# Kernel tuning notes

Measured on AMD Instinct MI355X. Metric: run time of the kernel, lower is better.

Reference implementation:

```python
import math
import jax, jax.numpy as jnp
import numpy as np

EPS_ATTN = 1e-8
LN_EPS = 1e-5


def layer_norm(x, g, b):
    mu = jnp.mean(x, axis=-1, keepdims=True)
    var = jnp.var(x, axis=-1, keepdims=True)
    return (x - mu) * jax.lax.rsqrt(var + LN_EPS) * g + b


def setup_inputs() -> dict:
    key = jax.random.key(0)
    ks = jax.random.split(key, 12)
    b, n, dim = 8, 8192, 384
    emb = 384
    m = int(emb * 0.5)  # 192 random features
    s = 0.02
    x = jax.random.normal(ks[0], (b, n, dim), dtype=jnp.float32)
    # fixed random-feature matrix (orthogonal*sqrt(m) in torch; random gaussian suffices as a baseline param)
    w = jax.random.normal(ks[1], (m, emb), dtype=jnp.float32) * math.sqrt(m) / math.sqrt(emb)
    # linear weights stored as [in, out] (torch Linear applies x @ W.T + b)
    kqv_w = jax.random.normal(ks[2], (dim, 3 * emb), dtype=jnp.float32) * s
    kqv_b = jax.random.normal(ks[3], (3 * emb,), dtype=jnp.float32) * s
    proj_w = jax.random.normal(ks[4], (emb, emb), dtype=jnp.float32) * s
    proj_b = jax.random.normal(ks[5], (emb,), dtype=jnp.float32) * s
    ln1_g = 1.0 + jax.random.normal(ks[6], (dim,), dtype=jnp.float32) * s
    ln1_b = jax.random.normal(ks[7], (dim,), dtype=jnp.float32) * s
    ln2_g = 1.0 + jax.random.normal(ks[8], (emb,), dtype=jnp.float32) * s
    ln2_b = jax.random.normal(ks[9], (emb,), dtype=jnp.float32) * s
    mlp_w1 = jax.random.normal(ks[10], (emb, emb), dtype=jnp.float32) * s
    mlp_b1 = jnp.zeros((emb,), dtype=jnp.float32)
    mlp_w2 = jax.random.normal(ks[11], (emb, emb), dtype=jnp.float32) * s
    mlp_b2 = jnp.zeros((emb,), dtype=jnp.float32)
    return {"x": x, "w": w, "kqv_w": kqv_w, "kqv_b": kqv_b, "proj_w": proj_w,
            "proj_b": proj_b, "ln1_g": ln1_g, "ln1_b": ln1_b, "ln2_g": ln2_g,
            "ln2_b": ln2_b, "mlp_w1": mlp_w1, "mlp_b1": mlp_b1,
            "mlp_w2": mlp_w2, "mlp_b2": mlp_b2}


def prm_exp(x, w):
    # FAVOR+ positive random features: exp(w @ x - |x|^2/2) / sqrt(m)
    m = w.shape[0]
    xd = 0.5 * jnp.sum(x * x, axis=-1, keepdims=True)          # [b, t, 1]
    wtx = jnp.einsum('bti,mi->btm', x, w)                       # [b, t, m]
    return jnp.exp(wtx - xd) / math.sqrt(m)


def reference(x, w, kqv_w, kqv_b, proj_w, proj_b, ln1_g, ln1_b,
              ln2_g, ln2_b, mlp_w1, mlp_b1, mlp_w2, mlp_b2):
    emb = proj_w.shape[0]
    h = layer_norm(x, ln1_g, ln1_b)
    kqv = h @ kqv_w + kqv_b                                     # [b, n, 3*emb]
    k, q, v = jnp.split(kqv, 3, axis=-1)
    kp = prm_exp(k, w)                                          # [b, n, m]
    qp = prm_exp(q, w)                                          # [b, n, m]
    D = jnp.einsum('btm,bm->bt', qp, kp.sum(axis=1))[..., None] # [b, n, 1]
    kptv = jnp.einsum('btn,btm->bnm', v, kp)                    # [b, emb, m]
    y = jnp.einsum('btm,bnm->btn', qp, kptv) / (D + EPS_ATTN)   # [b, n, emb]
    y = v + (y @ proj_w + proj_b)                               # residual (dropout=0)
    h2 = layer_norm(y, ln2_g, ln2_b)
    mlp = jax.nn.gelu(h2 @ mlp_w1 + mlp_b1, approximate=False) @ mlp_w2 + mlp_b2
    return y + mlp
```

## Files before the change

kernel.cpp:

```cpp
#include <hip/hip_runtime.h>
#include <cstdint>
#include <cstddef>


typedef __attribute__((ext_vector_type(8))) short s16x8;
typedef __attribute__((ext_vector_type(4))) short s16x4;
typedef __attribute__((ext_vector_type(4))) float fx4;
typedef __attribute__((ext_vector_type(8))) float fx8;

__device__ __forceinline__ float bf2f(short s) {
  union { float f; unsigned u; } z; z.u = ((unsigned)(unsigned short)s) << 16; return z.f;
}
__device__ __forceinline__ short f2bf(float f) {
  union { float f; unsigned u; } z; z.f = f;
  unsigned u = z.u;
  u += 0x7fffu + ((u >> 16) & 1u);
  return (short)(u >> 16);
}

__device__ __forceinline__ void mfma_bf16(fx4& d, s16x8 a, s16x8 b) {
  asm("v_mfma_f32_16x16x32_bf16 %0, %1, %2, %0" : "+v"(d) : "v"(a), "v"(b));
}

enum : int { M_BIAS=1, M_EXP=2, M_DIV=4, M_RESID=8, M_GELU=16, M_TSTORE=32,
             M_BATCHBT=64, M_KQVT=128, M_RESIDT=256, M_F32OUT=512 };

template<int BM, int BN, int MODE>
__global__ __launch_bounds__(256)
void gemm_tn(const short* __restrict__ A, int lda,
             const short* __restrict__ Bt, int ldbt, long btStride,
             short* __restrict__ C, int ldc,
             int K,
             const float* __restrict__ bias,
             const float* __restrict__ rowvec, float escale,
             const short* __restrict__ resid, int ldr, int rcol,
             short* __restrict__ vt)
{
  constexpr int WM = BM / 2, WN = BN / 2, MR = WM / 16, NR = WN / 16;
  constexpr int AIT = BM * 8 / 256, BIT = BN * 8 / 256;
  __shared__ __align__(16) short Al[BM][64];
  __shared__ __align__(16) short Bl[BN][64];

  const int tid = threadIdx.x;
  const int gx = gridDim.x;
  const int nwg = gx * gridDim.y;
  const int o = blockIdx.x + gx * blockIdx.y;
  const int swz = (o & 7) * (nwg >> 3) + (o >> 3);
  const int bx = swz % gx, by = swz / gx;
  const int row0 = by * BM, col0 = bx * BN;

  const short* Bt2 = (MODE & M_BATCHBT)
      ? Bt + (size_t)(row0 >> 13) * (size_t)btStride : Bt;
  const int w = tid >> 6, l = tid & 63;
  const int wr = w >> 1, wc = w & 1;
  const int lr = l & 15, lk = l >> 4;

  fx4 acc[MR][NR];
#pragma unroll
  for (int m = 0; m < MR; ++m)
#pragma unroll
    for (int n = 0; n < NR; ++n)
#pragma unroll
      for (int j = 0; j < 4; ++j) acc[m][n][j] = 0.0f;

  s16x8 areg[AIT], breg[BIT];

  auto loadA = [&](int kt) {
    const short* p = A + (size_t)row0 * lda + kt * 64;
#pragma unroll
    for (int i = 0; i < AIT; ++i) {
      int ch = i * 256 + tid;
      areg[i] = *(const s16x8*)(p + (size_t)(ch >> 3) * lda + ((ch & 7) * 8));
    }
  };
  auto loadB = [&](int kt) {
    const short* p = Bt2 + (size_t)col0 * ldbt + kt * 64;
#pragma unroll
    for (int i = 0; i < BIT; ++i) {
      int ch = i * 256 + tid;
      breg[i] = *(const s16x8*)(p + (size_t)(ch >> 3) * ldbt + ((ch & 7) * 8));
    }
  };
  auto storeA = [&]() {
#pragma unroll
    for (int i = 0; i < AIT; ++i) {
      int ch = i * 256 + tid, row = ch >> 3;
      *(s16x8*)&Al[row][((ch ^ row) & 7) * 8] = areg[i];
    }
  };
  auto storeB = [&]() {
#pragma unroll
    for (int i = 0; i < BIT; ++i) {
      int ch = i * 256 + tid, row = ch >> 3;
      *(s16x8*)&Bl[row][((ch ^ row) & 7) * 8] = breg[i];
    }
  };

  const int NT = K / 64;
  loadA(0); loadB(0); storeA(); storeB();
  __syncthreads();
  for (int kt = 0; kt < NT; ++kt) {
    if (kt + 1 < NT) { loadA(kt + 1); loadB(kt + 1); }
#pragma unroll
    for (int kk = 0; kk < 2; ++kk) {
      s16x8 af[MR], bfr[NR];
#pragma unroll
      for (int m = 0; m < MR; ++m) {
        const int ar = wr * WM + m * 16 + lr;
        af[m] = *(const s16x8*)&Al[ar][(((kk * 4 + lk) ^ ar) & 7) * 8];
      }
#pragma unroll
      for (int n = 0; n < NR; ++n) {
        const int br = wc * WN + n * 16 + lr;
        bfr[n] = *(const s16x8*)&Bl[br][(((kk * 4 + lk) ^ br) & 7) * 8];
      }
#pragma unroll
      for (int m = 0; m < MR; ++m)
#pragma unroll
        for (int n = 0; n < NR; ++n)
          mfma_bf16(acc[m][n], af[m], bfr[n]);
    }
    if (kt + 1 < NT) {
      __syncthreads();
      storeA(); storeB();
      __syncthreads();
    }
  }

#pragma unroll
  for (int m = 0; m < MR; ++m) {
#pragma unroll
    for (int n = 0; n < NR; ++n) {
      const int gcol = col0 + wc * WN + n * 16 + lr;
      const float bv = (MODE & M_BIAS) ? bias[gcol] : 0.0f;
#pragma unroll
      for (int j = 0; j < 4; ++j) {
        const int grow = row0 + wr * WM + m * 16 + lk * 4 + j;
        float v = acc[m][n][j] + bv;
        if (MODE & M_EXP)  v = expf(v - rowvec[grow]) * escale;
        if (MODE & M_DIV)  v = v / (rowvec[grow] + 1e-8f);
        if (MODE & M_GELU) v = 0.5f * v * (1.0f + erff(v * 0.70710678118654752f));
        if (MODE & M_RESID)  v += bf2f(resid[(size_t)grow * ldr + rcol + gcol]);
        if (MODE & M_RESIDT) v += bf2f(resid[((size_t)((grow >> 13) * ldr + gcol)) * 8192 + (grow & 8191)]);
        if (MODE & M_F32OUT) {
          ((float*)C)[(size_t)grow * ldc + gcol] = v;
        } else if (MODE & M_TSTORE) {
          C[((size_t)((grow >> 13) * ldc + gcol)) * 8192 + (grow & 8191)] = f2bf(v);
        } else if (MODE & M_KQVT) {
          if (gcol < 768) C[(size_t)grow * 768 + gcol] = f2bf(v);
          else vt[((size_t)((grow >> 13) * 384 + (gcol - 768))) * 8192 + (grow & 8191)] = f2bf(v);
        } else {
          C[(size_t)grow * ldc + gcol] = f2bf(v);
        }
      }
    }
  }
}

__global__ __launch_bounds__(256)
void gemm_kptv(const short* __restrict__ vT, const short* __restrict__ kpT,
               float* __restrict__ part)
{
  __shared__ __align__(16) short Al[128][64];
  __shared__ __align__(16) short Bl[64][64];
  const int tid = threadIdx.x;
  const int b = blockIdx.z >> 3, s = blockIdx.z & 7;
  const int row0 = blockIdx.x * 128, col0 = blockIdx.y * 64;
  const short* A  = vT  + ((size_t)(b * 384 + row0)) * 8192 + s * 1024;
  const short* Bt = kpT + ((size_t)(b * 192 + col0)) * 8192 + s * 1024;
  const int w = tid >> 6, l = tid & 63;
  const int wr = w >> 1, wc = w & 1, lr = l & 15, lk = l >> 4;

  fx4 acc[4][2];
#pragma unroll
  for (int m = 0; m < 4; ++m)
#pragma unroll
    for (int n = 0; n < 2; ++n)
#pragma unroll
      for (int j = 0; j < 4; ++j) acc[m][n][j] = 0.0f;

  s16x8 areg[4], breg[2];
  auto loadA = [&](int kt) {
#pragma unroll
    for (int i = 0; i < 4; ++i) {
      int ch = i * 256 + tid;
      areg[i] = *(const s16x8*)(A + kt * 64 + (size_t)(ch >> 3) * 8192 + ((ch & 7) * 8));
    }
  };
  auto loadB = [&](int kt) {
#pragma unroll
    for (int i = 0; i < 2; ++i) {
      int ch = i * 256 + tid;
      breg[i] = *(const s16x8*)(Bt + kt * 64 + (size_t)(ch >> 3) * 8192 + ((ch & 7) * 8));
    }
  };
  auto storeA = [&]() {
#pragma unroll
    for (int i = 0; i < 4; ++i) {
      int ch = i * 256 + tid, row = ch >> 3;
      *(s16x8*)&Al[row][((ch ^ row) & 7) * 8] = areg[i];
    }
  };
  auto storeB = [&]() {
#pragma unroll
    for (int i = 0; i < 2; ++i) {
      int ch = i * 256 + tid, row = ch >> 3;
      *(s16x8*)&Bl[row][((ch ^ row) & 7) * 8] = breg[i];
    }
  };

  loadA(0); loadB(0); storeA(); storeB();
  __syncthreads();
  for (int kt = 0; kt < 16; ++kt) {
    if (kt + 1 < 16) { loadA(kt + 1); loadB(kt + 1); }
#pragma unroll
    for (int kk = 0; kk < 2; ++kk) {
      s16x8 af[4], bfr[2];
#pragma unroll
      for (int m = 0; m < 4; ++m) {
        const int ar = wr * 64 + m * 16 + lr;
        af[m] = *(const s16x8*)&Al[ar][(((kk * 4 + lk) ^ ar) & 7) * 8];
      }
#pragma unroll
      for (int n = 0; n < 2; ++n) {
        const int br = wc * 32 + n * 16 + lr;
        bfr[n] = *(const s16x8*)&Bl[br][(((kk * 4 + lk) ^ br) & 7) * 8];
      }
#pragma unroll
      for (int m = 0; m < 4; ++m)
#pragma unroll
        for (int n = 0; n < 2; ++n)
          mfma_bf16(acc[m][n], af[m], bfr[n]);
    }
    if (kt + 1 < 16) {
      __syncthreads();
      storeA(); storeB();
      __syncthreads();
    }
  }

  float* outp = part + (size_t)blockIdx.z * 73728;
#pragma unroll
  for (int m = 0; m < 4; ++m)
#pragma unroll
    for (int n = 0; n < 2; ++n) {
      const int gm = col0 + wc * 32 + n * 16 + lr;
#pragma unroll
      for (int j = 0; j < 4; ++j) {
        const int gn = row0 + wr * 64 + m * 16 + lk * 4 + j;
        outp[(size_t)gn * 192 + gm] = acc[m][n][j];
      }
    }
}

__global__ void kptv_reduce(const float* __restrict__ part, short* __restrict__ outb)
{
  const int i = blockIdx.x * 256 + threadIdx.x;
  const int b = i / 73728, j = i - b * 73728;
  const float* p = part + (size_t)b * 8 * 73728 + j;
  float s = 0.0f;
#pragma unroll
  for (int k = 0; k < 8; ++k) s += p[(size_t)k * 73728];
  outb[i] = f2bf(s);
}

template<typename T>
__global__ __launch_bounds__(256)
void ln_kernel(const T* __restrict__ in, const float* __restrict__ g,
               const float* __restrict__ bta, short* __restrict__ out)
{
  const int tid = threadIdx.x, w = tid >> 6, l = tid & 63;
  const size_t t = (size_t)blockIdx.x * 4 + w;
  float x[8]; float sum = 0.0f, ss = 0.0f;
  const bool act = l < 48;
  if (act) {
    if constexpr (sizeof(T) == 2) {
      s16x8 v = *(const s16x8*)((const short*)in + t * 384 + l * 8);
#pragma unroll
      for (int i = 0; i < 8; ++i) x[i] = bf2f(v[i]);
    } else {
      fx8 v = *(const fx8*)((const float*)in + t * 384 + l * 8);
#pragma unroll
      for (int i = 0; i < 8; ++i) x[i] = v[i];
    }
#pragma unroll
    for (int i = 0; i < 8; ++i) { sum += x[i]; ss += x[i] * x[i]; }
  }
#pragma unroll
  for (int d = 1; d < 64; d <<= 1) { sum += __shfl_xor(sum, d); ss += __shfl_xor(ss, d); }
  const float mu = sum * (1.0f / 384.0f);
  const float rs = rsqrtf(ss * (1.0f / 384.0f) - mu * mu + 1e-5f);
  if (act) {
    fx8 gv = *(const fx8*)(g + l * 8);
    fx8 bv = *(const fx8*)(bta + l * 8);
    s16x8 o;
#pragma unroll
    for (int i = 0; i < 8; ++i) o[i] = f2bf((x[i] - mu) * rs * gv[i] + bv[i]);
    *(s16x8*)(out + t * 384 + l * 8) = o;
  }
}

__global__ __launch_bounds__(256)
void xd_kernel(const short* __restrict__ kq, float* __restrict__ xdk, float* __restrict__ xdq)
{
  const int tid = threadIdx.x, w = tid >> 6, l = tid & 63;
  const size_t t = (size_t)blockIdx.x * 2 + (w >> 1);
  const int half = w & 1;
  const short* row = kq + t * 768 + half * 384;
  float ss = 0.0f;
  if (l < 48) {
    s16x8 v = *(const s16x8*)(row + l * 8);
#pragma unroll
    for (int i = 0; i < 8; ++i) { float f = bf2f(v[i]); ss += f * f; }
  }
#pragma unroll
  for (int d = 1; d < 64; d <<= 1) ss += __shfl_xor(ss, d);
  if (l == 0) { (half ? xdq : xdk)[t] = 0.5f * ss; }
}

__global__ __launch_bounds__(256)
void rowsum_kernel(const short* __restrict__ kpT, float* __restrict__ sum)
{
  const int tid = threadIdx.x;
  const short* row = kpT + (size_t)blockIdx.x * 8192;
  float s = 0.0f;
  for (int i = tid; i < 1024; i += 256) {
    s16x8 v = ((const s16x8*)row)[i];
#pragma unroll
    for (int k = 0; k < 8; ++k) s += bf2f(v[k]);
  }
#pragma unroll
  for (int d = 1; d < 64; d <<= 1) s += __shfl_xor(s, d);
  __shared__ float ps[4];
  if ((tid & 63) == 0) ps[tid >> 6] = s;
  __syncthreads();
  if (tid == 0) sum[blockIdx.x] = ps[0] + ps[1] + ps[2] + ps[3];
}

__global__ __launch_bounds__(256)
void d_kernel(const short* __restrict__ qp, const float* __restrict__ kpsum,
              float* __restrict__ D)
{
  const int t = blockIdx.x * 256 + threadIdx.x;
  const int b = t >> 13;
  const short* row = qp + (size_t)t * 192;
  const float* ks = kpsum + b * 192;
  float acc = 0.0f;
#pragma unroll
  for (int j = 0; j < 24; ++j) {
    s16x8 v = ((const s16x8*)row)[j];
#pragma unroll
    for (int i = 0; i < 8; ++i) acc += bf2f(v[i]) * ks[j * 8 + i];
  }
  D[t] = acc;
}

__global__ void transpose_kernel(const float* __restrict__ src, short* __restrict__ dst,
                                 int R, int Cc)
{
  __shared__ float tile[32][33];
  const int c0 = blockIdx.x * 32, r0 = blockIdx.y * 32;
  for (int i = threadIdx.y; i < 32; i += 8)
    tile[i][threadIdx.x] = src[(size_t)(r0 + i) * Cc + c0 + threadIdx.x];
  __syncthreads();
  for (int i = threadIdx.y; i < 32; i += 8)
    dst[(size_t)(c0 + i) * R + r0 + threadIdx.x] = f2bf(tile[threadIdx.x][i]);
}

__global__ void convert_kernel(const float* __restrict__ src, short* __restrict__ dst)
{
  const int i = blockIdx.x * 1024 + threadIdx.x * 4;
  fx4 v = *(const fx4*)(src + i);
  s16x4 o;
#pragma unroll
  for (int k = 0; k < 4; ++k) o[k] = f2bf(v[k]);
  *(s16x4*)(dst + i) = o;
}

extern "C" void kernel_launch(void* const* d_in, const int* in_sizes, int n_in,
                              void* d_out, int out_size, void* d_ws, size_t ws_size,
                              hipStream_t stream)
{
  const float* x      = (const float*)d_in[0];
  const float* w      = (const float*)d_in[1];
  const float* kqv_w  = (const float*)d_in[2];
  const float* kqv_b  = (const float*)d_in[3];
  const float* proj_w = (const float*)d_in[4];
  const float* proj_b = (const float*)d_in[5];
  const float* ln1_g  = (const float*)d_in[6];
  const float* ln1_b  = (const float*)d_in[7];
  const float* ln2_g  = (const float*)d_in[8];
  const float* ln2_b  = (const float*)d_in[9];
  const float* w1     = (const float*)d_in[10];
  const float* b1     = (const float*)d_in[11];
  const float* w2     = (const float*)d_in[12];
  const float* b2     = (const float*)d_in[13];

  char* p = (char*)d_ws;
  auto take = [&](size_t n) { char* r = p; p += (n + 255) & ~(size_t)255; return r; };
  short* wtKQV  = (short*)take(1152 * 384 * 2);
  short* wtPROJ = (short*)take(384 * 384 * 2);
  short* wtM1   = (short*)take(384 * 384 * 2);
  short* wtM2   = (short*)take(384 * 384 * 2);
  short* wB     = (short*)take(192 * 384 * 2);
  short* KQ     = (short*)take((size_t)65536 * 768 * 2);
  short* VT     = (short*)take((size_t)8 * 384 * 8192 * 2);
  char*  KPQ    = take(50331648);
  float* XDK   = (float*)take(262144);
  float* XDQ   = (float*)take(262144);
  float* DV    = (float*)take(262144);
  float* KPSUM = (float*)take(1536 * 4);
  float* KPART = (float*)take((size_t)64 * 73728 * 4);
  short* KPTVB = (short*)take(1179648);

  short* H   = (short*)KPQ;
  short* KPT = (short*)KPQ;
  short* QP  = (short*)(KPQ + 25165824);
  short* Y   = (short*)KPQ;
  short* YA  = KQ;
  short* G   = KQ;
  short* H2  = VT;

  const float ESC = 0.07216878364870323f;
  dim3 blk(256);

  transpose_kernel<<<dim3(36, 12), dim3(32, 8), 0, stream>>>(kqv_w, wtKQV, 384, 1152);
  transpose_kernel<<<dim3(12, 12), dim3(32, 8), 0, stream>>>(proj_w, wtPROJ, 384, 384);
  transpose_kernel<<<dim3(12, 12), dim3(32, 8), 0, stream>>>(w1, wtM1, 384, 384);
  transpose_kernel<<<dim3(12, 12), dim3(32, 8), 0, stream>>>(w2, wtM2, 384, 384);
  convert_kernel<<<72, blk, 0, stream>>>(w, wB);

  ln_kernel<float><<<16384, blk, 0, stream>>>(x, ln1_g, ln1_b, H);

  gemm_tn<128, 128, M_BIAS | M_KQVT><<<dim3(9, 512), blk, 0, stream>>>(
      H, 384, wtKQV, 384, 0, KQ, 768, 384, kqv_b, nullptr, 0.f, nullptr, 0, 0, VT);

  xd_kernel<<<32768, blk, 0, stream>>>(KQ, XDK, XDQ);

  gemm_tn<128, 64, M_EXP | M_TSTORE><<<dim3(3, 512), blk, 0, stream>>>(
      KQ, 768, wB, 384, 0, KPT, 192, 384, nullptr, XDK, ESC, nullptr, 0, 0, nullptr);
  gemm_tn<128, 64, M_EXP><<<dim3(3, 512), blk, 0, stream>>>(
      KQ + 384, 768, wB, 384, 0, QP, 192, 384, nullptr, XDQ, ESC, nullptr, 0, 0, nullptr);

  rowsum_kernel<<<1536, blk, 0, stream>>>(KPT, KPSUM);
  d_kernel<<<256, blk, 0, stream>>>(QP, KPSUM, DV);

  gemm_kptv<<<dim3(3, 3, 64), blk, 0, stream>>>(VT, KPT, KPART);
  kptv_reduce<<<2304, blk, 0, stream>>>(KPART, KPTVB);

  gemm_tn<128, 128, M_DIV | M_BATCHBT><<<dim3(3, 512), blk, 0, stream>>>(
      QP, 192, KPTVB, 192, 73728, YA, 384, 192, nullptr, DV, 0.f, nullptr, 0, 0, nullptr);

  gemm_tn<128, 128, M_BIAS | M_RESIDT><<<dim3(3, 512), blk, 0, stream>>>(
      YA, 384, wtPROJ, 384, 0, Y, 384, 384, proj_b, nullptr, 0.f, VT, 384, 0, nullptr);

  ln_kernel<short><<<16384, blk, 0, stream>>>(Y, ln2_g, ln2_b, H2);

  gemm_tn<128, 128, M_BIAS | M_GELU><<<dim3(3, 512), blk, 0, stream>>>(
      H2, 384, wtM1, 384, 0, G, 384, 384, b1, nullptr, 0.f, nullptr, 0, 0, nullptr);

  gemm_tn<128, 128, M_BIAS | M_RESID | M_F32OUT><<<dim3(3, 512), blk, 0, stream>>>(
      G, 384, wtM2, 384, 0, (short*)d_out, 384, 384, b2, nullptr, 0.f, Y, 384, 0, nullptr);
}
```

Baseline: 502.9 us.

## Fuse LayerNorm2, MLP GEMM1+GELU and GEMM2+residual into one kernel

Replaces the second LayerNorm kernel and the two MLP GEMM launches with a single 512-thread kernel. Each block loads 64 rows of Y into shared memory, normalizes them, runs the first GEMM with GELU, keeps the hidden activations in LDS, then runs the second GEMM and adds the bias and residual. This removes the global round trips for H2 and G and two launches. In exchange it uses about 150KB of LDS per block, which limits occupancy, and launches only 1024 blocks with simple register-staged weight loading.

Result: slower. 518.1 us (+3.0%).

```diff
diff --git a/kernel.cpp b/kernel.cpp
--- a/kernel.cpp
+++ b/kernel.cpp
@@ -377,6 +377,154 @@
   *(s16x4*)(dst + i) = o;
 }
 
+__global__ __launch_bounds__(512)
+void mega2_kernel(const short* __restrict__ Y,
+                  const short* __restrict__ W1, const short* __restrict__ W2,
+                  const float* __restrict__ B1, const float* __restrict__ B2,
+                  const float* __restrict__ LG, const float* __restrict__ LB,
+                  float* __restrict__ out)
+{
+  __shared__ __align__(16) short Bl[384][72];
+  __shared__ __align__(16) short Ybuf[64][392];
+  __shared__ __align__(16) short Abuf[64][392];
+
+  const int tid = threadIdx.x;
+  const int w = tid >> 6, l = tid & 63;
+  const int wr = w & 1, wc = w >> 1;
+  const int lr = l & 15, lk = l >> 4;
+  const int t0 = blockIdx.x * 64;
+
+  fx4 acc[2][6];
+  s16x8 breg[6];
+
+  auto zacc = [&]() {
+#pragma unroll
+    for (int m = 0; m < 2; ++m)
+#pragma unroll
+      for (int n = 0; n < 6; ++n)
+#pragma unroll
+        for (int j = 0; j < 4; ++j) acc[m][n][j] = 0.0f;
+  };
+  auto loadB6 = [&](const short* W, int kt) {
+#pragma unroll
+    for (int p = 0; p < 6; ++p) {
+      int lin = p * 512 + tid;
+      breg[p] = *(const s16x8*)(W + (size_t)(lin >> 3) * 384 + kt * 64 + (lin & 7) * 8);
+    }
+  };
+  auto storeB6 = [&]() {
+#pragma unroll
+    for (int p = 0; p < 6; ++p) {
+      int lin = p * 512 + tid;
+      *(s16x8*)&Bl[lin >> 3][(lin & 7) * 8] = breg[p];
+    }
+  };
+
+#pragma unroll
+  for (int p = 0; p < 6; ++p) {
+    int lin = p * 512 + tid;
+    int r = lin / 48, c = (lin % 48) * 8;
+    *(s16x8*)&Ybuf[r][c] = *(const s16x8*)(Y + (size_t)(t0 + r) * 384 + c);
+  }
+  __syncthreads();
+
+  {
+    const int r = tid >> 3, seg = tid & 7;
+    float xv[48]; float sum = 0.0f, ss = 0.0f;
+#pragma unroll
+    for (int j2 = 0; j2 < 6; ++j2) {
+      s16x8 vv = *(const s16x8*)&Ybuf[r][seg * 48 + j2 * 8];
+#pragma unroll
+      for (int i = 0; i < 8; ++i) { float f = bf2f(vv[i]); xv[j2 * 8 + i] = f; sum += f; ss += f * f; }
+    }
+    sum += __shfl_xor(sum, 1); sum += __shfl_xor(sum, 2); sum += __shfl_xor(sum, 4);
+    ss  += __shfl_xor(ss, 1);  ss  += __shfl_xor(ss, 2);  ss  += __shfl_xor(ss, 4);
+    const float mu = sum * (1.0f / 384.0f);
+    const float rs = rsqrtf(ss * (1.0f / 384.0f) - mu * mu + 1e-5f);
+#pragma unroll
+    for (int j2 = 0; j2 < 6; ++j2) {
+      fx4 g0 = *(const fx4*)(LG + seg * 48 + j2 * 8);
+      fx4 g1 = *(const fx4*)(LG + seg * 48 + j2 * 8 + 4);
+      fx4 b0 = *(const fx4*)(LB + seg * 48 + j2 * 8);
+      fx4 b1v = *(const fx4*)(LB + seg * 48 + j2 * 8 + 4);
+      s16x8 o;
+#pragma unroll
+      for (int i = 0; i < 4; ++i) o[i] = f2bf((xv[j2 * 8 + i] - mu) * rs * g0[i] + b0[i]);
+#pragma unroll
+      for (int i = 0; i < 4; ++i) o[4 + i] = f2bf((xv[j2 * 8 + 4 + i] - mu) * rs * g1[i] + b1v[i]);
+      *(s16x8*)&Abuf[r][seg * 48 + j2 * 8] = o;
+    }
+  }
+  __syncthreads();
+
+  zacc();
+  loadB6(W1, 0);
+  for (int kt = 0; kt < 6; ++kt) {
+    __syncthreads();
+    storeB6();
+    if (kt < 5) loadB6(W1, kt + 1);
+    __syncthreads();
+#pragma unroll
+    for (int k2 = 0; k2 < 2; ++k2) {
+      s16x8 af0 = *(const s16x8*)&Abuf[wr * 32 + lr][kt * 64 + k2 * 32 + lk * 8];
+      s16x8 af1 = *(const s16x8*)&Abuf[wr * 32 + 16 + lr][kt * 64 + k2 * 32 + lk * 8];
+#pragma unroll
+      for (int n = 0; n < 6; ++n) {
+        s16x8 bfr = *(const s16x8*)&Bl[wc * 96 + n * 16 + lr][k2 * 32 + lk * 8];
+        mfma_bf16(acc[0][n], af0, bfr);
+        mfma_bf16(acc[1][n], af1, bfr);
+      }
+    }
+  }
+  __syncthreads();
+#pragma unroll
+  for (int m = 0; m < 2; ++m)
+#pragma unroll
+    for (int n = 0; n < 6; ++n) {
+      const int ccol = wc * 96 + n * 16 + lr;
+      const float bb = B1[ccol];
+#pragma unroll
+      for (int j = 0; j < 4; ++j) {
+        const int crow = wr * 32 + m * 16 + lk * 4 + j;
+        float v = acc[m][n][j] + bb;
+        v = 0.5f * v * (1.0f + erff(v * 0.70710678118654752f));
+        Abuf[crow][ccol] = f2bf(v);
+      }
+    }
+
+  zacc();
+  loadB6(W2, 0);
+  for (int kt = 0; kt < 6; ++kt) {
+    __syncthreads();
+    storeB6();
+    if (kt < 5) loadB6(W2, kt + 1);
+    __syncthreads();
+#pragma unroll
+    for (int k2 = 0; k2 < 2; ++k2) {
+      s16x8 af0 = *(const s16x8*)&Abuf[wr * 32 + lr][kt * 64 + k2 * 32 + lk * 8];
+      s16x8 af1 = *(const s16x8*)&Abuf[wr * 32 + 16 + lr][kt * 64 + k2 * 32 + lk * 8];
+#pragma unroll
+      for (int n = 0; n < 6; ++n) {
+        s16x8 bfr = *(const s16x8*)&Bl[wc * 96 + n * 16 + lr][k2 * 32 + lk * 8];
+        mfma_bf16(acc[0][n], af0, bfr);
+        mfma_bf16(acc[1][n], af1, bfr);
+      }
+    }
+  }
+#pragma unroll
+  for (int m = 0; m < 2; ++m)
+#pragma unroll
+    for (int n = 0; n < 6; ++n) {
+      const int ccol = wc * 96 + n * 16 + lr;
+      const float bb = B2[ccol];
+#pragma unroll
+      for (int j = 0; j < 4; ++j) {
+        const int crow = wr * 32 + m * 16 + lk * 4 + j;
+        out[(size_t)(t0 + crow) * 384 + ccol] = acc[m][n][j] + bb + bf2f(Ybuf[crow][ccol]);
+      }
+    }
+}
+
 extern "C" void kernel_launch(void* const* d_in, const int* in_sizes, int n_in,
                               void* d_out, int out_size, void* d_ws, size_t ws_size,
                               hipStream_t stream)
@@ -418,8 +566,6 @@
   short* QP  = (short*)(KPQ + 25165824);
   short* Y   = (short*)KPQ;
   short* YA  = KQ;
-  short* G   = KQ;
-  short* H2  = VT;
 
   const float ESC = 0.07216878364870323f;
   dim3 blk(256);
@@ -454,11 +600,6 @@
   gemm_tn<128, 128, M_BIAS | M_RESIDT><<<dim3(3, 512), blk, 0, stream>>>(
       YA, 384, wtPROJ, 384, 0, Y, 384, 384, proj_b, nullptr, 0.f, VT, 384, 0, nullptr);
 
-  ln_kernel<short><<<16384, blk, 0, stream>>>(Y, ln2_g, ln2_b, H2);
-
-  gemm_tn<128, 128, M_BIAS | M_GELU><<<dim3(3, 512), blk, 0, stream>>>(
-      H2, 384, wtM1, 384, 0, G, 384, 384, b1, nullptr, 0.f, nullptr, 0, 0, nullptr);
-
-  gemm_tn<128, 128, M_BIAS | M_RESID | M_F32OUT><<<dim3(3, 512), blk, 0, stream>>>(
-      G, 384, wtM2, 384, 0, (short*)d_out, 384, 384, b2, nullptr, 0.f, Y, 384, 0, nullptr);
-}
+  mega2_kernel<<<1024, dim3(512), 0, stream>>>(
+      Y, wtM1, wtM2, b1, b2, ln2_g, ln2_b, (float*)d_out);
+}
```

## Fuse row-norm and denominator reductions into GEMM A-tile loads

Applied to the files above, without the earlier changes.

Computes the per-row half squared norm of k/q inside the random-feature GEMMs as the A tiles are loaded. It also computes the denominator dot product with the key-feature sums inside the attention-output GEMM's A loads. This removes the separate xd_kernel and d_kernel launches and their extra full reads of KQ and QP. In exchange it adds per-thread FMA work, shuffles, an extra barrier and shared storage in the GEMM epilogue, and the norm is recomputed in each of the three column blocks.

Measured after the change: 486.4 us. 3.3% less time.

```diff
diff --git a/kernel.cpp b/kernel.cpp
--- a/kernel.cpp
+++ b/kernel.cpp
@@ -23,7 +23,8 @@
 }
 
 enum : int { M_BIAS=1, M_EXP=2, M_DIV=4, M_RESID=8, M_GELU=16, M_TSTORE=32,
-             M_BATCHBT=64, M_KQVT=128, M_RESIDT=256, M_F32OUT=512 };
+             M_BATCHBT=64, M_KQVT=128, M_RESIDT=256, M_F32OUT=512,
+             M_XA=1024, M_DOTB=2048 };
 
 template<int BM, int BN, int MODE>
 __global__ __launch_bounds__(256)
@@ -40,6 +41,7 @@
   constexpr int AIT = BM * 8 / 256, BIT = BN * 8 / 256;
   __shared__ __align__(16) short Al[BM][64];
   __shared__ __align__(16) short Bl[BN][64];
+  __shared__ float xdl[(MODE & (M_XA | M_DOTB)) ? BM : 1];
 
   const int tid = threadIdx.x;
   const int gx = gridDim.x;
@@ -64,6 +66,9 @@
       for (int j = 0; j < 4; ++j) acc[m][n][j] = 0.0f;
 
   s16x8 areg[AIT], breg[BIT];
+  float xacc[(MODE & (M_XA | M_DOTB)) ? AIT : 1];
+#pragma unroll
+  for (int i = 0; i < (int)(sizeof(xacc) / sizeof(float)); ++i) xacc[i] = 0.0f;
 
   auto loadA = [&](int kt) {
     const short* p = A + (size_t)row0 * lda + kt * 64;
@@ -71,6 +76,15 @@
     for (int i = 0; i < AIT; ++i) {
       int ch = i * 256 + tid;
       areg[i] = *(const s16x8*)(p + (size_t)(ch >> 3) * lda + ((ch & 7) * 8));
+      if (MODE & M_XA) {
+#pragma unroll
+        for (int jj = 0; jj < 8; ++jj) { float f = bf2f(areg[i][jj]); xacc[i] += f * f; }
+      }
+      if (MODE & M_DOTB) {
+        const float* dv = rowvec + (row0 >> 13) * 192 + kt * 64 + (ch & 7) * 8;
+#pragma unroll
+        for (int jj = 0; jj < 8; ++jj) xacc[i] += bf2f(areg[i][jj]) * dv[jj];
+      }
     }
   };
   auto loadB = [&](int kt) {
@@ -127,6 +141,16 @@
     }
   }
 
+  if (MODE & (M_XA | M_DOTB)) {
+#pragma unroll
+    for (int i = 0; i < (int)(sizeof(xacc) / sizeof(float)); ++i) {
+      float s = xacc[i];
+      s += __shfl_xor(s, 1); s += __shfl_xor(s, 2); s += __shfl_xor(s, 4);
+      if ((tid & 7) == 0) xdl[i * 32 + (tid >> 3)] = (MODE & M_XA) ? 0.5f * s : s;
+    }
+    __syncthreads();
+  }
+
 #pragma unroll
   for (int m = 0; m < MR; ++m) {
 #pragma unroll
@@ -135,10 +159,11 @@
       const float bv = (MODE & M_BIAS) ? bias[gcol] : 0.0f;
 #pragma unroll
       for (int j = 0; j < 4; ++j) {
-        const int grow = row0 + wr * WM + m * 16 + lk * 4 + j;
+        const int lrow = wr * WM + m * 16 + lk * 4 + j;
+        const int grow = row0 + lrow;
         float v = acc[m][n][j] + bv;
-        if (MODE & M_EXP)  v = expf(v - rowvec[grow]) * escale;
-        if (MODE & M_DIV)  v = v / (rowvec[grow] + 1e-8f);
+        if (MODE & M_EXP)  v = expf(v - xdl[lrow]) * escale;
+        if (MODE & M_DIV)  v = v / (xdl[lrow] + 1e-8f);
         if (MODE & M_GELU) v = 0.5f * v * (1.0f + erff(v * 0.70710678118654752f));
         if (MODE & M_RESID)  v += bf2f(resid[(size_t)grow * ldr + rcol + gcol]);
         if (MODE & M_RESIDT) v += bf2f(resid[((size_t)((grow >> 13) * ldr + gcol)) * 8192 + (grow & 8191)]);
@@ -301,24 +326,6 @@
 }
 
 __global__ __launch_bounds__(256)
-void xd_kernel(const short* __restrict__ kq, float* __restrict__ xdk, float* __restrict__ xdq)
-{
-  const int tid = threadIdx.x, w = tid >> 6, l = tid & 63;
-  const size_t t = (size_t)blockIdx.x * 2 + (w >> 1);
-  const int half = w & 1;
-  const short* row = kq + t * 768 + half * 384;
-  float ss = 0.0f;
-  if (l < 48) {
-    s16x8 v = *(const s16x8*)(row + l * 8);
-#pragma unroll
-    for (int i = 0; i < 8; ++i) { float f = bf2f(v[i]); ss += f * f; }
-  }
-#pragma unroll
-  for (int d = 1; d < 64; d <<= 1) ss += __shfl_xor(ss, d);
-  if (l == 0) { (half ? xdq : xdk)[t] = 0.5f * ss; }
-}
-
-__global__ __launch_bounds__(256)
 void rowsum_kernel(const short* __restrict__ kpT, float* __restrict__ sum)
 {
   const int tid = threadIdx.x;
@@ -335,24 +342,6 @@
   if ((tid & 63) == 0) ps[tid >> 6] = s;
   __syncthreads();
   if (tid == 0) sum[blockIdx.x] = ps[0] + ps[1] + ps[2] + ps[3];
-}
-
-__global__ __launch_bounds__(256)
-void d_kernel(const short* __restrict__ qp, const float* __restrict__ kpsum,
-              float* __restrict__ D)
-{
-  const int t = blockIdx.x * 256 + threadIdx.x;
-  const int b = t >> 13;
-  const short* row = qp + (size_t)t * 192;
-  const float* ks = kpsum + b * 192;
-  float acc = 0.0f;
-#pragma unroll
-  for (int j = 0; j < 24; ++j) {
-    s16x8 v = ((const s16x8*)row)[j];
-#pragma unroll
-    for (int i = 0; i < 8; ++i) acc += bf2f(v[i]) * ks[j * 8 + i];
-  }
-  D[t] = acc;
 }
 
 __global__ void transpose_kernel(const float* __restrict__ src, short* __restrict__ dst,
@@ -406,9 +395,6 @@
   short* KQ     = (short*)take((size_t)65536 * 768 * 2);
   short* VT     = (short*)take((size_t)8 * 384 * 8192 * 2);
   char*  KPQ    = take(50331648);
-  float* XDK   = (float*)take(262144);
-  float* XDQ   = (float*)take(262144);
-  float* DV    = (float*)take(262144);
   float* KPSUM = (float*)take(1536 * 4);
   float* KPART = (float*)take((size_t)64 * 73728 * 4);
   short* KPTVB = (short*)take(1179648);
@@ -435,21 +421,18 @@
   gemm_tn<128, 128, M_BIAS | M_KQVT><<<dim3(9, 512), blk, 0, stream>>>(
       H, 384, wtKQV, 384, 0, KQ, 768, 384, kqv_b, nullptr, 0.f, nullptr, 0, 0, VT);
 
-  xd_kernel<<<32768, blk, 0, stream>>>(KQ, XDK, XDQ);
-
-  gemm_tn<128, 64, M_EXP | M_TSTORE><<<dim3(3, 512), blk, 0, stream>>>(
-      KQ, 768, wB, 384, 0, KPT, 192, 384, nullptr, XDK, ESC, nullptr, 0, 0, nullptr);
-  gemm_tn<128, 64, M_EXP><<<dim3(3, 512), blk, 0, stream>>>(
-      KQ + 384, 768, wB, 384, 0, QP, 192, 384, nullptr, XDQ, ESC, nullptr, 0, 0, nullptr);
+  gemm_tn<128, 64, M_EXP | M_TSTORE | M_XA><<<dim3(3, 512), blk, 0, stream>>>(
+      KQ, 768, wB, 384, 0, KPT, 192, 384, nullptr, nullptr, ESC, nullptr, 0, 0, nullptr);
+  gemm_tn<128, 64, M_EXP | M_XA><<<dim3(3, 512), blk, 0, stream>>>(
+      KQ + 384, 768, wB, 384, 0, QP, 192, 384, nullptr, nullptr, ESC, nullptr, 0, 0, nullptr);
 
   rowsum_kernel<<<1536, blk, 0, stream>>>(KPT, KPSUM);
-  d_kernel<<<256, blk, 0, stream>>>(QP, KPSUM, DV);
 
   gemm_kptv<<<dim3(3, 3, 64), blk, 0, stream>>>(VT, KPT, KPART);
   kptv_reduce<<<2304, blk, 0, stream>>>(KPART, KPTVB);
 
-  gemm_tn<128, 128, M_DIV | M_BATCHBT><<<dim3(3, 512), blk, 0, stream>>>(
-      QP, 192, KPTVB, 192, 73728, YA, 384, 192, nullptr, DV, 0.f, nullptr, 0, 0, nullptr);
+  gemm_tn<128, 128, M_DIV | M_BATCHBT | M_DOTB><<<dim3(3, 512), blk, 0, stream>>>(
+      QP, 192, KPTVB, 192, 73728, YA, 384, 192, nullptr, KPSUM, 0.f, nullptr, 0, 0, nullptr);
 
   gemm_tn<128, 128, M_BIAS | M_RESIDT><<<dim3(3, 512), blk, 0, stream>>>(
       YA, 384, wtPROJ, 384, 0, Y, 384, 384, proj_b, nullptr, 0.f, VT, 384, 0, nullptr);
```
